# Optimization experiments

Hardware: AMD Instinct MI355X
Metric: run time of the kernel (lower is better)

The kernel has to match this reference:

```python
import jax, jax.numpy as jnp
import numpy as np
from math import exp, log

# Instant-NGP style multi-hash-grid constants (match init_kwargs)
BASE_RES = 16
MAX_RES = 2048
N_GRIDS = 16
LOG2_T = 19
TABLE_SIZE = 1 << LOG2_T  # power of two -> mod == low-bit mask
FEAT = 2
N_POINTS = 1_000_000

_pls = exp((log(MAX_RES) - log(BASE_RES)) / (N_GRIDS - 1))
RESOLUTIONS = np.floor(np.array([BASE_RES * _pls ** i for i in range(N_GRIDS)])).astype(np.float32)
# 8 voxel corner offsets, i-major (i*4 + j*2 + k) like the torch VOXEL_VTX_OFFSET
OFFSETS = np.array([[i, j, k] for i in (0, 1) for j in (0, 1) for k in (0, 1)], dtype=np.int32)
PRIMES = np.array([1, 2654435761, 805459861], dtype=np.uint32)


def setup_inputs() -> dict:
    key = jax.random.key(0)
    k1, k2 = jax.random.split(key)
    x = jax.random.normal(k1, (N_POINTS, 3), dtype=jnp.float32)
    # nn.init.uniform_(weight, a=-1e-4, b=1e-4)
    tables = jax.random.uniform(k2, (N_GRIDS, TABLE_SIZE, FEAT),
                                minval=-1e-4, maxval=1e-4, dtype=jnp.float32)
    return {"x": x, "tables": tables}


def _forward(x, tables):
    inbox = jnp.all((x >= -1.0) & (x <= 1.0), axis=-1)  # [B]
    offs = jnp.asarray(OFFSETS)                          # [8,3]
    primes = jnp.asarray(PRIMES)                         # [3] uint32
    res = jnp.asarray(RESOLUTIONS)                       # [G]
    # torch computes x_normed / interp weights under no_grad -> no grad to x
    xs = jax.lax.stop_gradient(x)

    def level(table, r):
        # (x - bbox_min) / (bbox_max - bbox_min) * resolution, bbox = [-1,1]^3
        xn = (xs + 1.0) * 0.5 * r                        # [B,3]
        v0 = jnp.floor(xn).astype(jnp.int32)             # [B,3]
        w = xn - v0.astype(jnp.float32)                  # [B,3] trilerp weights
        vidx = (v0[:, None, :] + offs[None]).astype(jnp.uint32)  # [B,8,3]
        # prime-XOR spatial hash; uint32 wraparound matches torch int64 math
        # modulo the power-of-two table size (low bits identical)
        h = (vidx[..., 0] * primes[0]) ^ (vidx[..., 1] * primes[1]) ^ (vidx[..., 2] * primes[2])
        h = (h & jnp.uint32(TABLE_SIZE - 1)).astype(jnp.int32)   # [B,8]
        feats = table[h]                                  # [B,8,F] gather
        # corner (i,j,k) weight = prod over dims of (w if bit else 1-w)
        wgt = jnp.prod(jnp.where(offs[None] == 1, w[:, None, :], 1.0 - w[:, None, :]), axis=-1)  # [B,8]
        c = jnp.einsum('bc,bcf->bf', wgt, feats)          # [B,F]
        return jnp.where(inbox[:, None], c, 0.0)          # out-of-bbox -> zeros

    per_level = jax.vmap(level)(tables, res)              # [G,B,F]
    B = x.shape[0]
    return jnp.transpose(per_level, (1, 0, 2)).reshape(B, N_GRIDS * FEAT)


def reference(x, tables):
    return _forward(x, tables)
```

## Files before the change

kernel.cpp:

```cpp
#include <hip/hip_runtime.h>
#include <hip/hip_bf16.h>
#include <math.h>

#define N_POINTS 1000000
#define N_GRIDS  16
#define LOG2_T   19
#define TABLE_MASK ((1u << LOG2_T) - 1u)
#define NBLOCKS  ((N_POINTS + 255) / 256)
#define CONV_BLOCKS 4096
#define FUSED_BLOCKS 2048
#define TAILB_BLOCKS 4096
#define N_ENTRIES (N_GRIDS << LOG2_T)
#define NCELL_AX 32
#define N_CELLS  (NCELL_AX * NCELL_AX * NCELL_AX)

struct ResArr { float r[N_GRIDS]; };

__device__ __forceinline__ unsigned pack_bf16x2(float a, float b)
{
    __hip_bfloat16 ha = __float2bfloat16(a);
    __hip_bfloat16 hb = __float2bfloat16(b);
    unsigned short ua = *(unsigned short*)&ha;
    unsigned short ub = *(unsigned short*)&hb;
    return (unsigned)ua | ((unsigned)ub << 16);
}

__device__ __forceinline__ float2 unpack_bf16x2(unsigned v)
{
    unsigned lo = (v & 0xffffu) << 16;
    unsigned hi = v & 0xffff0000u;
    return make_float2(__uint_as_float(lo), __uint_as_float(hi));
}

__device__ __forceinline__ unsigned expand_bits(unsigned v)
{
    v &= 0x3ffu;
    v = (v | (v << 16)) & 0x30000FFu;
    v = (v | (v << 8))  & 0x300F00Fu;
    v = (v | (v << 4))  & 0x30C30C3u;
    v = (v | (v << 2))  & 0x9249249u;
    return v;
}

__device__ __forceinline__ int morton_cell(float x0, float x1, float x2)
{
    int cx = (int)floorf((x0 + 1.f) * 16.f);
    int cy = (int)floorf((x1 + 1.f) * 16.f);
    int cz = (int)floorf((x2 + 1.f) * 16.f);
    cx = min(NCELL_AX - 1, max(0, cx));
    cy = min(NCELL_AX - 1, max(0, cy));
    cz = min(NCELL_AX - 1, max(0, cz));
    return (int)((expand_bits((unsigned)cx) << 2) |
                 (expand_bits((unsigned)cy) << 1) |
                  expand_bits((unsigned)cz));
}

__device__ __forceinline__ void gather_level_bf16(
    float x0, float x1, float x2, float r,
    const unsigned* __restrict__ tbl, float& c0, float& c1)
{
    const float xn0 = (x0 + 1.0f) * 0.5f * r;
    const float xn1 = (x1 + 1.0f) * 0.5f * r;
    const float xn2 = (x2 + 1.0f) * 0.5f * r;
    const float f0 = floorf(xn0), f1 = floorf(xn1), f2 = floorf(xn2);
    const unsigned v0 = (unsigned)(int)f0;
    const unsigned v1 = (unsigned)(int)f1;
    const unsigned v2 = (unsigned)(int)f2;
    const float w0 = xn0 - f0, w1 = xn1 - f1, w2 = xn2 - f2;

    unsigned fv[8];
    #pragma unroll
    for (int k = 0; k < 8; ++k) {
        const unsigned vx = v0 + ((k >> 2) & 1);
        const unsigned vy = v1 + ((k >> 1) & 1);
        const unsigned vz = v2 + (k & 1);
        unsigned h = vx ^ (vy * 2654435761u) ^ (vz * 805459861u);
        fv[k] = tbl[h & TABLE_MASK];
    }
    c0 = 0.f; c1 = 0.f;
    #pragma unroll
    for (int k = 0; k < 8; ++k) {
        const float wgt = ((k & 4) ? w0 : 1.0f - w0) *
                          ((k & 2) ? w1 : 1.0f - w1) *
                          ((k & 1) ? w2 : 1.0f - w2);
        const float2 f = unpack_bf16x2(fv[k]);
        c0 += wgt * f.x;
        c1 += wgt * f.y;
    }
}

__global__ __launch_bounds__(256)
void hist_conv_kernel(const float* __restrict__ x, int* __restrict__ rank,
                      unsigned* __restrict__ hist,
                      const float* __restrict__ tables,
                      unsigned* __restrict__ tb)
{
    if (blockIdx.x < NBLOCKS) {
        const int p = blockIdx.x * 256 + threadIdx.x;
        if (p >= N_POINTS) return;
        const float x0 = x[3 * p], x1 = x[3 * p + 1], x2 = x[3 * p + 2];
        const bool inbox = (x0 >= -1.f) & (x0 <= 1.f) &
                           (x1 >= -1.f) & (x1 <= 1.f) &
                           (x2 >= -1.f) & (x2 <= 1.f);
        if (inbox) {
            const int cell = morton_cell(x0, x1, x2);
            atomicAdd(&hist[cell], 1u);
            rank[p] = cell;
        } else {
            rank[p] = -1;
        }
    } else {
        const unsigned nthr = CONV_BLOCKS * 256;
        for (unsigned e4 = (blockIdx.x - NBLOCKS) * 256 + threadIdx.x;
             e4 < (N_ENTRIES / 4); e4 += nthr) {
            const float4 a = ((const float4*)tables)[2 * e4];
            const float4 b = ((const float4*)tables)[2 * e4 + 1];
            uint4 o;
            o.x = pack_bf16x2(a.x, a.y);
            o.y = pack_bf16x2(a.z, a.w);
            o.z = pack_bf16x2(b.x, b.y);
            o.w = pack_bf16x2(b.z, b.w);
            ((uint4*)tb)[e4] = o;
        }
    }
}

__global__ __launch_bounds__(1024)
void scan_kernel(unsigned* __restrict__ hist, unsigned* __restrict__ counter)
{
    __shared__ unsigned partial[1024];
    const int tid = threadIdx.x;
    uint4* __restrict__ hp = (uint4*)hist + tid * 8;
    uint4 vv[8];
    unsigned s = 0;
    #pragma unroll
    for (int i = 0; i < 8; ++i) {
        vv[i] = hp[i];
        s += vv[i].x + vv[i].y + vv[i].z + vv[i].w;
    }
    partial[tid] = s;
    __syncthreads();
    for (int off = 1; off < 1024; off <<= 1) {
        unsigned t = (tid >= off) ? partial[tid - off] : 0u;
        __syncthreads();
        partial[tid] += t;
        __syncthreads();
    }
    if (tid == 1023) counter[0] = partial[1023];
    unsigned run = partial[tid] - s;
    #pragma unroll
    for (int i = 0; i < 8; ++i) {
        uint4 o;
        o.x = run; run += vv[i].x;
        o.y = run; run += vv[i].y;
        o.z = run; run += vv[i].z;
        o.w = run; run += vv[i].w;
        hp[i] = o;
    }
}

__global__ __launch_bounds__(256)
void scatter_kernel(const float* __restrict__ x, int* __restrict__ rank,
                    float4* __restrict__ xw, unsigned* __restrict__ hist)
{
    const int p = blockIdx.x * 256 + threadIdx.x;
    if (p >= N_POINTS) return;
    const int cell = rank[p];
    if (cell < 0) return;
    const unsigned rk = atomicAdd(&hist[cell], 1u);
    rank[p] = (int)rk;
    xw[rk] = make_float4(x[3 * p], x[3 * p + 1], x[3 * p + 2],
                         __int_as_float(p));
}

__global__ __launch_bounds__(256)
void fused_levels_kernel(const float4* __restrict__ xw,
                         const unsigned* __restrict__ counter,
                         const unsigned* __restrict__ tb,
                         unsigned* __restrict__ ws2, ResArr res,
                         const int* __restrict__ rank,
                         float* __restrict__ out)
{
    if (blockIdx.x < FUSED_BLOCKS) {
        const unsigned k    = blockIdx.x & 7;
        const unsigned bix  = blockIdx.x >> 3;
        const unsigned nbx  = FUSED_BLOCKS >> 3;
        const unsigned cnt  = *counter;
        const unsigned per  = (cnt + nbx - 1) / nbx;
        const unsigned lo   = bix * per;
        const unsigned hi   = min(cnt, lo + per);

        #pragma unroll 1
        for (int t = 0; t < 2; ++t) {
            const int g = t ? (15 - (int)k) : (int)k;
            const float r = res.r[g];
            const unsigned* __restrict__ tbl = tb + ((size_t)g << LOG2_T);
            unsigned* __restrict__ wrow = ws2 + (size_t)g * N_POINTS;
            for (unsigned i = lo + threadIdx.x; i < hi; i += 256) {
                const float4 v = xw[i];
                float c0, c1;
                gather_level_bf16(v.x, v.y, v.z, r, tbl, c0, c1);
                wrow[i] = pack_bf16x2(c0, c1);
            }
        }
    } else {
        const unsigned zb = blockIdx.x - FUSED_BLOCKS;
        const int P0 = (int)zb * 256;
        float4* __restrict__ out4 = (float4*)out + (size_t)P0 * 8;
        const float4 z = make_float4(0.f, 0.f, 0.f, 0.f);
        const int t = threadIdx.x;
        #pragma unroll
        for (int i = 0; i < 8; ++i) {
            const int j  = i * 256 + t;
            const int pp = P0 + (j >> 3);
            if (pp < N_POINTS && rank[pp] < 0) out4[j] = z;
        }
    }
}

__global__ __launch_bounds__(256)
void tail_kernel(const float4* __restrict__ xw,
                 const unsigned* __restrict__ counter,
                 const unsigned* __restrict__ ws2, float* __restrict__ out)
{
    const int t = threadIdx.x;
    const unsigned cnt = *counter;
    const unsigned tot = cnt * 8u;
    for (unsigned tg = blockIdx.x * 256 + t; tg < tot;
         tg += TAILB_BLOCKS * 256) {
        const unsigned i = tg >> 3, q = tg & 7;
        const unsigned a = ws2[(size_t)(2 * q) * N_POINTS + i];
        const unsigned b = ws2[(size_t)(2 * q + 1) * N_POINTS + i];
        const int p = __float_as_int(xw[i].w);
        const float2 fa = unpack_bf16x2(a);
        const float2 fb = unpack_bf16x2(b);
        ((float4*)out)[(size_t)p * 8 + q] =
            make_float4(fa.x, fa.y, fb.x, fb.y);
    }
}

__device__ __forceinline__ void gather_level_f32(
    float x0, float x1, float x2, float r,
    const float2* __restrict__ tbl, float& c0, float& c1)
{
    const float xn0 = (x0 + 1.0f) * 0.5f * r;
    const float xn1 = (x1 + 1.0f) * 0.5f * r;
    const float xn2 = (x2 + 1.0f) * 0.5f * r;
    const float f0 = floorf(xn0), f1 = floorf(xn1), f2 = floorf(xn2);
    const unsigned v0 = (unsigned)(int)f0;
    const unsigned v1 = (unsigned)(int)f1;
    const unsigned v2 = (unsigned)(int)f2;
    const float w0 = xn0 - f0, w1 = xn1 - f1, w2 = xn2 - f2;
    c0 = 0.f; c1 = 0.f;
    #pragma unroll
    for (int k = 0; k < 8; ++k) {
        const unsigned vx = v0 + ((k >> 2) & 1);
        const unsigned vy = v1 + ((k >> 1) & 1);
        const unsigned vz = v2 + (k & 1);
        unsigned h = (vx * 1u) ^ (vy * 2654435761u) ^ (vz * 805459861u);
        h &= TABLE_MASK;
        const float wgt = ((k & 4) ? w0 : 1.0f - w0) *
                          ((k & 2) ? w1 : 1.0f - w1) *
                          ((k & 1) ? w2 : 1.0f - w2);
        const float2 f = tbl[h];
        c0 += wgt * f.x;
        c1 += wgt * f.y;
    }
}

__global__ __launch_bounds__(256)
void mono_kernel(const float* __restrict__ x, const float* __restrict__ tables,
                 float* __restrict__ out, ResArr res)
{
    int idx = blockIdx.x * blockDim.x + threadIdx.x;
    if (idx >= N_POINTS * N_GRIDS) return;
    int b = idx >> 4, g = idx & 15;
    float x0 = x[b * 3], x1 = x[b * 3 + 1], x2 = x[b * 3 + 2];
    bool inbox = (x0 >= -1.f) & (x0 <= 1.f) & (x1 >= -1.f) & (x1 <= 1.f) &
                 (x2 >= -1.f) & (x2 <= 1.f);
    float c0 = 0.f, c1 = 0.f;
    if (inbox) {
        const float2* tbl = (const float2*)tables + ((size_t)g << LOG2_T);
        gather_level_f32(x0, x1, x2, res.r[g], tbl, c0, c1);
    }
    ((float2*)out)[(size_t)b * N_GRIDS + g] = make_float2(c0, c1);
}

extern "C" void kernel_launch(void* const* d_in, const int* in_sizes, int n_in,
                              void* d_out, int out_size, void* d_ws, size_t ws_size,
                              hipStream_t stream)
{
    const float* x      = (const float*)d_in[0];
    const float* tables = (const float*)d_in[1];
    float* out          = (float*)d_out;

    ResArr res;
    double pls = exp((log(2048.0) - log(16.0)) / 15.0);
    for (int i = 0; i < N_GRIDS; ++i)
        res.r[i] = (float)floor(16.0 * pow(pls, (double)i));

    const size_t off_hist = 256;
    const size_t off_rank = off_hist + (size_t)N_CELLS * 4;
    const size_t off_xw   = off_rank + (size_t)N_POINTS * 4;
    const size_t off_ws2  = off_xw + (size_t)N_POINTS * 16;
    const size_t off_tb   = off_ws2 + (size_t)N_GRIDS * N_POINTS * 4;
    const size_t ws_needed = off_tb + (size_t)N_ENTRIES * 4;

    if (ws_size < ws_needed) {
        int total = N_POINTS * N_GRIDS;
        mono_kernel<<<(total + 255) / 256, 256, 0, stream>>>(x, tables, out, res);
        return;
    }

    char* w = (char*)d_ws;
    unsigned* counter = (unsigned*)w;
    unsigned* hist    = (unsigned*)(w + off_hist);
    int*      rank    = (int*)(w + off_rank);
    float4*   xw      = (float4*)(w + off_xw);
    unsigned* ws2     = (unsigned*)(w + off_ws2);
    unsigned* tb      = (unsigned*)(w + off_tb);

    (void)hipMemsetAsync(w, 0, off_rank, stream);
    hist_conv_kernel<<<NBLOCKS + CONV_BLOCKS, 256, 0, stream>>>(
        x, rank, hist, tables, tb);
    scan_kernel<<<1, 1024, 0, stream>>>(hist, counter);
    scatter_kernel<<<NBLOCKS, 256, 0, stream>>>(x, rank, xw, hist);
    fused_levels_kernel<<<FUSED_BLOCKS + NBLOCKS, 256, 0, stream>>>(
        xw, counter, tb, ws2, res, rank, out);
    tail_kernel<<<TAILB_BLOCKS, 256, 0, stream>>>(xw, counter, ws2, out);
}
```

Before: 198.4 us.

## Pair x-adjacent hash corners into single 8-byte loads; move zero-fill to tail kernel

The x-neighbour corners differ in their hash only by v0^(v0+1). When that xor is 1 the two corners share an aligned 8-byte pair, so the gather loads uint2 and picks a half by the low bit, which allows fewer distinct cache lines per lookup. The zero-fill of out-of-box rows moves from the gather kernel into the tail kernel, so the gather launch runs only compute blocks. The risks are twice the load width for corners that do not share a pair, and a longer tail kernel.

```diff
diff --git a/kernel.cpp b/kernel.cpp
--- a/kernel.cpp
+++ b/kernel.cpp
@@ -57,7 +57,7 @@
 
 __device__ __forceinline__ void gather_level_bf16(
     float x0, float x1, float x2, float r,
-    const unsigned* __restrict__ tbl, float& c0, float& c1)
+    const uint2* __restrict__ tbl2, float& c0, float& c1)
 {
     const float xn0 = (x0 + 1.0f) * 0.5f * r;
     const float xn1 = (x1 + 1.0f) * 0.5f * r;
@@ -67,25 +67,36 @@
     const unsigned v1 = (unsigned)(int)f1;
     const unsigned v2 = (unsigned)(int)f2;
     const float w0 = xn0 - f0, w1 = xn1 - f1, w2 = xn2 - f2;
-
-    unsigned fv[8];
-    #pragma unroll
-    for (int k = 0; k < 8; ++k) {
-        const unsigned vx = v0 + ((k >> 2) & 1);
-        const unsigned vy = v1 + ((k >> 1) & 1);
-        const unsigned vz = v2 + (k & 1);
-        unsigned h = vx ^ (vy * 2654435761u) ^ (vz * 805459861u);
-        fv[k] = tbl[h & TABLE_MASK];
+    const unsigned d = v0 ^ (v0 + 1u);
+
+    uint2 pv[8];
+    unsigned sel[8];
+    #pragma unroll
+    for (int yz = 0; yz < 4; ++yz) {
+        const unsigned vy = v1 + ((yz >> 1) & 1);
+        const unsigned vz = v2 + (yz & 1);
+        const unsigned m  = (vy * 2654435761u) ^ (vz * 805459861u);
+        const unsigned sa = (v0 ^ m) & TABLE_MASK;
+        const unsigned sb = (sa ^ d) & TABLE_MASK;
+        pv[2 * yz]      = tbl2[sa >> 1];
+        pv[2 * yz + 1]  = tbl2[sb >> 1];
+        sel[2 * yz]     = sa & 1u;
+        sel[2 * yz + 1] = sb & 1u;
     }
     c0 = 0.f; c1 = 0.f;
     #pragma unroll
-    for (int k = 0; k < 8; ++k) {
-        const float wgt = ((k & 4) ? w0 : 1.0f - w0) *
-                          ((k & 2) ? w1 : 1.0f - w1) *
-                          ((k & 1) ? w2 : 1.0f - w2);
-        const float2 f = unpack_bf16x2(fv[k]);
-        c0 += wgt * f.x;
-        c1 += wgt * f.y;
+    for (int yz = 0; yz < 4; ++yz) {
+        const float wy  = (yz & 2) ? w1 : 1.0f - w1;
+        const float wz  = (yz & 1) ? w2 : 1.0f - w2;
+        const float wyz = wy * wz;
+        const unsigned ua = sel[2 * yz]     ? pv[2 * yz].y     : pv[2 * yz].x;
+        const unsigned ub = sel[2 * yz + 1] ? pv[2 * yz + 1].y : pv[2 * yz + 1].x;
+        const float2 fa = unpack_bf16x2(ua);
+        const float2 fb = unpack_bf16x2(ub);
+        const float wa = (1.0f - w0) * wyz;
+        const float wb = w0 * wyz;
+        c0 += wa * fa.x; c1 += wa * fa.y;
+        c0 += wb * fb.x; c1 += wb * fb.y;
     }
 }
 
@@ -177,65 +188,62 @@
 void fused_levels_kernel(const float4* __restrict__ xw,
                          const unsigned* __restrict__ counter,
                          const unsigned* __restrict__ tb,
-                         unsigned* __restrict__ ws2, ResArr res,
-                         const int* __restrict__ rank,
-                         float* __restrict__ out)
-{
-    if (blockIdx.x < FUSED_BLOCKS) {
-        const unsigned k    = blockIdx.x & 7;
-        const unsigned bix  = blockIdx.x >> 3;
-        const unsigned nbx  = FUSED_BLOCKS >> 3;
-        const unsigned cnt  = *counter;
-        const unsigned per  = (cnt + nbx - 1) / nbx;
-        const unsigned lo   = bix * per;
-        const unsigned hi   = min(cnt, lo + per);
-
-        #pragma unroll 1
-        for (int t = 0; t < 2; ++t) {
-            const int g = t ? (15 - (int)k) : (int)k;
-            const float r = res.r[g];
-            const unsigned* __restrict__ tbl = tb + ((size_t)g << LOG2_T);
-            unsigned* __restrict__ wrow = ws2 + (size_t)g * N_POINTS;
-            for (unsigned i = lo + threadIdx.x; i < hi; i += 256) {
-                const float4 v = xw[i];
-                float c0, c1;
-                gather_level_bf16(v.x, v.y, v.z, r, tbl, c0, c1);
-                wrow[i] = pack_bf16x2(c0, c1);
-            }
-        }
-    } else {
-        const unsigned zb = blockIdx.x - FUSED_BLOCKS;
-        const int P0 = (int)zb * 256;
+                         unsigned* __restrict__ ws2, ResArr res)
+{
+    const unsigned k    = blockIdx.x & 7;
+    const unsigned bix  = blockIdx.x >> 3;
+    const unsigned nbx  = gridDim.x >> 3;
+    const unsigned cnt  = *counter;
+    const unsigned per  = (cnt + nbx - 1) / nbx;
+    const unsigned lo   = bix * per;
+    const unsigned hi   = min(cnt, lo + per);
+
+    #pragma unroll 1
+    for (int t = 0; t < 2; ++t) {
+        const int g = t ? (15 - (int)k) : (int)k;
+        const float r = res.r[g];
+        const uint2* __restrict__ tbl2 =
+            (const uint2*)(tb + ((size_t)g << LOG2_T));
+        unsigned* __restrict__ wrow = ws2 + (size_t)g * N_POINTS;
+        for (unsigned i = lo + threadIdx.x; i < hi; i += 256) {
+            const float4 v = xw[i];
+            float c0, c1;
+            gather_level_bf16(v.x, v.y, v.z, r, tbl2, c0, c1);
+            wrow[i] = pack_bf16x2(c0, c1);
+        }
+    }
+}
+
+__global__ __launch_bounds__(256)
+void tail_kernel(const int* __restrict__ rank, const float4* __restrict__ xw,
+                 const unsigned* __restrict__ counter,
+                 const unsigned* __restrict__ ws2, float* __restrict__ out)
+{
+    const int t = threadIdx.x;
+    if (blockIdx.x < NBLOCKS) {
+        const int P0 = blockIdx.x * 256;
         float4* __restrict__ out4 = (float4*)out + (size_t)P0 * 8;
         const float4 z = make_float4(0.f, 0.f, 0.f, 0.f);
-        const int t = threadIdx.x;
         #pragma unroll
         for (int i = 0; i < 8; ++i) {
             const int j  = i * 256 + t;
             const int pp = P0 + (j >> 3);
             if (pp < N_POINTS && rank[pp] < 0) out4[j] = z;
         }
-    }
-}
-
-__global__ __launch_bounds__(256)
-void tail_kernel(const float4* __restrict__ xw,
-                 const unsigned* __restrict__ counter,
-                 const unsigned* __restrict__ ws2, float* __restrict__ out)
-{
-    const int t = threadIdx.x;
-    const unsigned cnt = *counter;
-    const unsigned tot = cnt * 8u;
-    for (unsigned tg = blockIdx.x * 256 + t; tg < tot;
-         tg += TAILB_BLOCKS * 256) {
-        const unsigned i = tg >> 3, q = tg & 7;
-        const unsigned a = ws2[(size_t)(2 * q) * N_POINTS + i];
-        const unsigned b = ws2[(size_t)(2 * q + 1) * N_POINTS + i];
-        const int p = __float_as_int(xw[i].w);
-        const float2 fa = unpack_bf16x2(a);
-        const float2 fb = unpack_bf16x2(b);
-        ((float4*)out)[(size_t)p * 8 + q] =
-            make_float4(fa.x, fa.y, fb.x, fb.y);
+    } else {
+        const unsigned cnt = *counter;
+        const unsigned tot = cnt * 8u;
+        const unsigned bix = blockIdx.x - NBLOCKS;
+        for (unsigned tg = bix * 256 + t; tg < tot; tg += TAILB_BLOCKS * 256) {
+            const unsigned i = tg >> 3, q = tg & 7;
+            const unsigned a = ws2[(size_t)(2 * q) * N_POINTS + i];
+            const unsigned b = ws2[(size_t)(2 * q + 1) * N_POINTS + i];
+            const int p = __float_as_int(xw[i].w);
+            const float2 fa = unpack_bf16x2(a);
+            const float2 fb = unpack_bf16x2(b);
+            ((float4*)out)[(size_t)p * 8 + q] =
+                make_float4(fa.x, fa.y, fb.x, fb.y);
+        }
     }
 }
 
@@ -325,7 +333,8 @@
         x, rank, hist, tables, tb);
     scan_kernel<<<1, 1024, 0, stream>>>(hist, counter);
     scatter_kernel<<<NBLOCKS, 256, 0, stream>>>(x, rank, xw, hist);
-    fused_levels_kernel<<<FUSED_BLOCKS + NBLOCKS, 256, 0, stream>>>(
-        xw, counter, tb, ws2, res, rank, out);
-    tail_kernel<<<TAILB_BLOCKS, 256, 0, stream>>>(xw, counter, ws2, out);
-}
+    fused_levels_kernel<<<FUSED_BLOCKS, 256, 0, stream>>>(xw, counter, tb,
+                                                          ws2, res);
+    tail_kernel<<<NBLOCKS + TAILB_BLOCKS, 256, 0, stream>>>(rank, xw, counter,
+                                                            ws2, out);
+}
```

Measured after the change: 202.1 us. About the same (+1.9%).

## Rebalance level work across block groups via host task table; move zero-fill to tail

Applied to the files above, without the earlier changes.

Replaces the fixed pairing of levels (k and 15-k) per block group with a host-built task table that assigns whole coarse levels and fractional slices of the two finest levels to each of 8 groups, aiming to equalize per-group gather cost. The zero-fill of out-of-box points moves from the levels kernel into the tail kernel. The goal is to reduce load imbalance where fine levels with scattered hash lookups dominate. The cut points are hand-tuned and may not match actual per-level costs.

```diff
diff --git a/kernel.cpp b/kernel.cpp
--- a/kernel.cpp
+++ b/kernel.cpp
@@ -15,6 +15,8 @@
 #define N_CELLS  (NCELL_AX * NCELL_AX * NCELL_AX)
 
 struct ResArr { float r[N_GRIDS]; };
+struct Task    { int g, lo, hi; };
+struct TaskTab { Task t[8][6]; int n[8]; };
 
 __device__ __forceinline__ unsigned pack_bf16x2(float a, float b)
 {
@@ -177,65 +179,68 @@
 void fused_levels_kernel(const float4* __restrict__ xw,
                          const unsigned* __restrict__ counter,
                          const unsigned* __restrict__ tb,
-                         unsigned* __restrict__ ws2, ResArr res,
-                         const int* __restrict__ rank,
-                         float* __restrict__ out)
-{
-    if (blockIdx.x < FUSED_BLOCKS) {
-        const unsigned k    = blockIdx.x & 7;
-        const unsigned bix  = blockIdx.x >> 3;
-        const unsigned nbx  = FUSED_BLOCKS >> 3;
-        const unsigned cnt  = *counter;
-        const unsigned per  = (cnt + nbx - 1) / nbx;
-        const unsigned lo   = bix * per;
-        const unsigned hi   = min(cnt, lo + per);
-
-        #pragma unroll 1
-        for (int t = 0; t < 2; ++t) {
-            const int g = t ? (15 - (int)k) : (int)k;
-            const float r = res.r[g];
-            const unsigned* __restrict__ tbl = tb + ((size_t)g << LOG2_T);
-            unsigned* __restrict__ wrow = ws2 + (size_t)g * N_POINTS;
-            for (unsigned i = lo + threadIdx.x; i < hi; i += 256) {
-                const float4 v = xw[i];
-                float c0, c1;
-                gather_level_bf16(v.x, v.y, v.z, r, tbl, c0, c1);
-                wrow[i] = pack_bf16x2(c0, c1);
-            }
-        }
-    } else {
-        const unsigned zb = blockIdx.x - FUSED_BLOCKS;
-        const int P0 = (int)zb * 256;
+                         unsigned* __restrict__ ws2, ResArr res, TaskTab tt)
+{
+    const unsigned k    = blockIdx.x & 7;
+    const unsigned bix  = blockIdx.x >> 3;
+    const unsigned nbx  = gridDim.x >> 3;
+    const unsigned cnt  = *counter;
+
+    #pragma unroll 1
+    for (int tix = 0; tix < tt.n[k]; ++tix) {
+        const int g = tt.t[k][tix].g;
+        const unsigned lo =
+            (unsigned)(((unsigned long long)tt.t[k][tix].lo * cnt) >> 8);
+        const unsigned hi =
+            (unsigned)(((unsigned long long)tt.t[k][tix].hi * cnt) >> 8);
+        const unsigned len = hi - lo;
+        if (!len) continue;
+        const unsigned per = (len + nbx - 1) / nbx;
+        const unsigned s0  = lo + bix * per;
+        const unsigned s1  = min(hi, s0 + per);
+
+        const float r = res.r[g];
+        const unsigned* __restrict__ tbl = tb + ((size_t)g << LOG2_T);
+        unsigned* __restrict__ wrow = ws2 + (size_t)g * N_POINTS;
+        for (unsigned i = s0 + threadIdx.x; i < s1; i += 256) {
+            const float4 v = xw[i];
+            float c0, c1;
+            gather_level_bf16(v.x, v.y, v.z, r, tbl, c0, c1);
+            wrow[i] = pack_bf16x2(c0, c1);
+        }
+    }
+}
+
+__global__ __launch_bounds__(256)
+void tail_kernel(const int* __restrict__ rank, const float4* __restrict__ xw,
+                 const unsigned* __restrict__ counter,
+                 const unsigned* __restrict__ ws2, float* __restrict__ out)
+{
+    const int t = threadIdx.x;
+    if (blockIdx.x < NBLOCKS) {
+        const int P0 = blockIdx.x * 256;
         float4* __restrict__ out4 = (float4*)out + (size_t)P0 * 8;
         const float4 z = make_float4(0.f, 0.f, 0.f, 0.f);
-        const int t = threadIdx.x;
         #pragma unroll
         for (int i = 0; i < 8; ++i) {
             const int j  = i * 256 + t;
             const int pp = P0 + (j >> 3);
             if (pp < N_POINTS && rank[pp] < 0) out4[j] = z;
         }
-    }
-}
-
-__global__ __launch_bounds__(256)
-void tail_kernel(const float4* __restrict__ xw,
-                 const unsigned* __restrict__ counter,
-                 const unsigned* __restrict__ ws2, float* __restrict__ out)
-{
-    const int t = threadIdx.x;
-    const unsigned cnt = *counter;
-    const unsigned tot = cnt * 8u;
-    for (unsigned tg = blockIdx.x * 256 + t; tg < tot;
-         tg += TAILB_BLOCKS * 256) {
-        const unsigned i = tg >> 3, q = tg & 7;
-        const unsigned a = ws2[(size_t)(2 * q) * N_POINTS + i];
-        const unsigned b = ws2[(size_t)(2 * q + 1) * N_POINTS + i];
-        const int p = __float_as_int(xw[i].w);
-        const float2 fa = unpack_bf16x2(a);
-        const float2 fb = unpack_bf16x2(b);
-        ((float4*)out)[(size_t)p * 8 + q] =
-            make_float4(fa.x, fa.y, fb.x, fb.y);
+    } else {
+        const unsigned cnt = *counter;
+        const unsigned tot = cnt * 8u;
+        const unsigned bix = blockIdx.x - NBLOCKS;
+        for (unsigned tg = bix * 256 + t; tg < tot; tg += TAILB_BLOCKS * 256) {
+            const unsigned i = tg >> 3, q = tg & 7;
+            const unsigned a = ws2[(size_t)(2 * q) * N_POINTS + i];
+            const unsigned b = ws2[(size_t)(2 * q + 1) * N_POINTS + i];
+            const int p = __float_as_int(xw[i].w);
+            const float2 fa = unpack_bf16x2(a);
+            const float2 fb = unpack_bf16x2(b);
+            ((float4*)out)[(size_t)p * 8 + q] =
+                make_float4(fa.x, fa.y, fb.x, fb.y);
+        }
     }
 }
 
@@ -299,6 +304,35 @@
     for (int i = 0; i < N_GRIDS; ++i)
         res.r[i] = (float)floor(16.0 * pow(pls, (double)i));
 
+    TaskTab tt;
+    for (int k = 0; k < 8; ++k) tt.n[k] = 0;
+    auto add = [&](int grp, int g, int lo, int hi) {
+        tt.t[grp][tt.n[grp]].g  = g;
+        tt.t[grp][tt.n[grp]].lo = lo;
+        tt.t[grp][tt.n[grp]].hi = hi;
+        tt.n[grp]++;
+    };
+    for (int k = 0; k < 7; ++k) add(k, 7 + k, 0, 256);
+    add(0, 4, 0, 256);
+    const int cuts[8] = {0, 36, 116, 195, 274, 353, 432, 512};
+    for (int k = 0; k < 7; ++k) {
+        int a = cuts[k], b = cuts[k + 1];
+        if (a < 256 && b > 0) {
+            int lo = a, hi = b < 256 ? b : 256;
+            if (lo < hi) add(k, 14, lo, hi);
+        }
+        if (b > 256) {
+            int lo = a > 256 ? a - 256 : 0, hi = b - 256;
+            if (lo < hi) add(k, 15, lo, hi);
+        }
+    }
+    add(7, 6, 0, 256);
+    add(7, 5, 0, 256);
+    add(7, 3, 0, 256);
+    add(7, 2, 0, 256);
+    add(7, 1, 0, 256);
+    add(7, 0, 0, 256);
+
     const size_t off_hist = 256;
     const size_t off_rank = off_hist + (size_t)N_CELLS * 4;
     const size_t off_xw   = off_rank + (size_t)N_POINTS * 4;
@@ -325,7 +359,8 @@
         x, rank, hist, tables, tb);
     scan_kernel<<<1, 1024, 0, stream>>>(hist, counter);
     scatter_kernel<<<NBLOCKS, 256, 0, stream>>>(x, rank, xw, hist);
-    fused_levels_kernel<<<FUSED_BLOCKS + NBLOCKS, 256, 0, stream>>>(
-        xw, counter, tb, ws2, res, rank, out);
-    tail_kernel<<<TAILB_BLOCKS, 256, 0, stream>>>(xw, counter, ws2, out);
-}
+    fused_levels_kernel<<<FUSED_BLOCKS, 256, 0, stream>>>(xw, counter, tb,
+                                                          ws2, res, tt);
+    tail_kernel<<<NBLOCKS + TAILB_BLOCKS, 256, 0, stream>>>(rank, xw, counter,
+                                                            ws2, out);
+}
```

Result: slower. 220.8 us (+11.3%).
